# Optimization experiments

Measured on AMD Instinct MI355X. Metric: run time of the kernel, lower is better.

The kernel has to match this reference:

```python
import math
import jax, jax.numpy as jnp
import numpy as np

B, P, L = 32, 128, 64
DIN, TE, H, NH, NL = 16, 64, 512, 8, 2
DH = H // NH
DP = DIN + TE
TAU = 300.0
DELTA = 300.0

_PARAM_SPEC = [
    ("te_scale_w", (1, 1)), ("te_scale_b", (1,)),
    ("te_per_w", (TE - 1, 1)), ("te_per_b", (TE - 1,)),
    ("inp_w", (H, DP)), ("inp_b", (H,)),
    ("wq", (H, H)), ("bq", (H,)), ("wk", (H, H)), ("bk", (H,)),
    ("wv", (H, H)), ("bv", (H,)), ("wo", (H, H)), ("bo", (H,)),
    ("ffn_w1", (H, H)), ("ffn_b1", (H,)), ("ffn_w2", (H, H)), ("ffn_b2", (H,)),
    ("ln1_g", (H,)), ("ln1_b", (H,)), ("ln2_g", (H,)), ("ln2_b", (H,)),
    ("exists_bias", (1, 1, H)),
    ("gwq", (NL, H, H)), ("gbq", (NL, H)), ("gwk", (NL, H, H)), ("gbk", (NL, H)),
    ("gwv", (NL, H, H)), ("gbv", (NL, H)), ("gwo", (NL, H, H)), ("gbo", (NL, H)),
]


def setup_inputs() -> dict:
    key = jax.random.key(0)
    ks = jax.random.split(key, 3 + len(_PARAM_SPEC))
    inp = {
        "x": jax.random.normal(ks[0], (B, P, L, DIN), jnp.float32),
        "tt": jax.random.uniform(ks[1], (B, P, L, 1), jnp.float32),
        "mask": jax.random.randint(ks[2], (B, P, L, 1), 0, 2).astype(jnp.int32),
    }
    for i, (name, shp) in enumerate(_PARAM_SPEC):
        inp[name] = 0.02 * jax.random.normal(ks[3 + i], shp, jnp.float32)
    # LayerNorm affine params: gamma=1, beta=0
    inp["ln1_g"] = jnp.ones((H,), jnp.float32)
    inp["ln1_b"] = jnp.zeros((H,), jnp.float32)
    inp["ln2_g"] = jnp.ones((H,), jnp.float32)
    inp["ln2_b"] = jnp.zeros((H,), jnp.float32)
    return inp


def _layernorm(x, g, b, eps=1e-5):
    m = x.mean(-1, keepdims=True)
    v = ((x - m) ** 2).mean(-1, keepdims=True)
    return (x - m) / jnp.sqrt(v + eps) * g + b


def _time_bias(m):
    idx = jnp.arange(m)
    dist = jnp.abs(idx[:, None] - idx[None, :]).astype(jnp.float32) * DELTA
    return jnp.log(jnp.exp(-dist / TAU) + 1e-12)  # [P, P]


def _pos_encoding(p, d):
    pos = jnp.arange(p, dtype=jnp.float32)[:, None]
    div = jnp.exp(jnp.arange(0, d, 2, dtype=jnp.float32) * (-math.log(10000.0) / d))
    pe = jnp.zeros((p, d), jnp.float32)
    pe = pe.at[:, 0::2].set(jnp.sin(pos * div))
    pe = pe.at[:, 1::2].set(jnp.cos(pos * div))
    return pe


def reference(x, tt, mask,
              te_scale_w, te_scale_b, te_per_w, te_per_b,
              inp_w, inp_b, wq, bq, wk, bk, wv, bv, wo, bo,
              ffn_w1, ffn_b1, ffn_w2, ffn_b2, ln1_g, ln1_b, ln2_g, ln2_b,
              exists_bias, gwq, gbq, gwk, gbk, gwv, gbv, gwo, gbo):
    b, p, l, _ = x.shape
    # --- Learnable time embedding: scale linear + sin(periodic linear), concat ---
    te1 = tt @ te_scale_w.T + te_scale_b                      # [B,P,L,1]
    te2 = jnp.sin(tt @ te_per_w.T + te_per_b)                 # [B,P,L,TE-1]
    pts = jnp.concatenate([x, te1, te2], axis=-1)             # [B,P,L,DP]

    valid = (mask[..., 0] > 0).reshape(b * p, l)              # [N,L] bool
    h = (pts.reshape(b * p, l, DP) @ inp_w.T) + inp_b         # [N,L,H]

    has_any = jnp.any(valid, axis=1)                          # [N]
    key_pad = ~valid
    # Empty patches: unmask position 0 and zero its features
    key_pad = key_pad.at[:, 0].set(key_pad[:, 0] & has_any)
    pos0 = (jnp.arange(l) == 0)[None, :, None]
    h = jnp.where((~has_any)[:, None, None] & pos0, 0.0, h)

    # --- Intra-patch MHA (GAT) ---
    def heads(t, w, bias):
        return ((t @ w.T) + bias).reshape(b * p, l, NH, DH)
    q, k, v = heads(h, wq, bq), heads(h, wk, bk), heads(h, wv, bv)
    sc = jnp.einsum("nqhd,nkhd->nhqk", q, k) / math.sqrt(DH)
    sc = jnp.where(key_pad[:, None, None, :], -1e9, sc)
    z = jnp.einsum("nhqk,nkhd->nqhd", jax.nn.softmax(sc, axis=-1), v)
    z = z.reshape(b * p, l, H) @ wo.T + bo
    h = _layernorm(h + z, ln1_g, ln1_b)
    ffn = jax.nn.relu(h @ ffn_w1.T + ffn_b1) @ ffn_w2.T + ffn_b2
    h = _layernorm(h + ffn, ln2_g, ln2_b)

    # Masked mean pooling -> patch tokens
    w = valid.astype(jnp.float32)[..., None]                  # [N,L,1]
    denom = jnp.clip(w.sum(axis=1), 1.0)
    h = ((h * w).sum(axis=1) / denom).reshape(b, p, H)        # [B,P,H]

    # Exists bias for missing patches + positional encoding
    pexists = has_any.reshape(b, p).astype(jnp.float32)       # [B,P]
    h = h + exists_bias * (1.0 - pexists)[..., None]
    h = h + _pos_encoding(p, H)[None]

    # --- Patch-level time-biased graph attention stack (residual) ---
    tb = _time_bias(p)[None, None]                            # [1,1,P,P]
    kp = (pexists <= 0.0)[:, None, None, :]                   # [B,1,1,P]
    for li in range(NL):
        def gh(t, w, bias):
            return ((t @ w.T) + bias).reshape(b, p, NH, DH)
        q = gh(h, gwq[li], gbq[li])
        k = gh(h, gwk[li], gbk[li])
        v = gh(h, gwv[li], gbv[li])
        att = jnp.einsum("bqhd,bkhd->bhqk", q, k) / math.sqrt(DH) + tb
        att = jnp.where(kp, -1e9, att)
        out = jnp.einsum("bhqk,bkhd->bqhd", jax.nn.softmax(att, axis=-1), v)
        out = out.reshape(b, p, H) @ gwo[li].T + gbo[li]
        out = out * pexists[..., None]
        h = h + out
    return h
```

## Files before the change

### kernel.cpp

```cpp
#include <hip/hip_runtime.h>

#define NTOK 4096
#define CH   512
#define NCHUNK 8

typedef _Float16 f16;
typedef __attribute__((ext_vector_type(8))) _Float16 half8;
typedef __attribute__((ext_vector_type(4))) _Float16 half4;
typedef __attribute__((ext_vector_type(4))) float f32x4;

#define OFF_INPW 0
#define OFF_WQKV (512*128)
#define OFF_WO   (OFF_WQKV + 3*512*512)
#define OFF_W1   (OFF_WO + 512*512)
#define OFF_W2   (OFF_W1 + 512*512)
#define OFF_GW   (OFF_W2 + 512*512)
#define WBF_TOT  (OFF_GW + 8*512*512)

static __device__ __forceinline__ f32x4 mfma16(half8 a, half8 b, f32x4 c){
  return __builtin_amdgcn_mfma_f32_16x16x32_f16(a, b, c, 0, 0, 0);
}

static __device__ __forceinline__ void gld_lds16(const f16* g, f16* l){
  __builtin_amdgcn_global_load_lds(
      (const __attribute__((address_space(1))) void*)g,
      (__attribute__((address_space(3))) void*)l, 16, 0, 0);
}

#define FULL_BARRIER() do { \
    asm volatile("" ::: "memory"); \
    __builtin_amdgcn_s_barrier(); \
    __builtin_amdgcn_sched_barrier(0); \
  } while(0)

__global__ __launch_bounds__(256) void conv_weights(
    const float* __restrict__ inpw, const float* __restrict__ wq, const float* __restrict__ wk,
    const float* __restrict__ wv, const float* __restrict__ wo, const float* __restrict__ w1,
    const float* __restrict__ w2, const float* __restrict__ gwq, const float* __restrict__ gwk,
    const float* __restrict__ gwv, const float* __restrict__ gwo, f16* __restrict__ wbf,
    const float* __restrict__ bq, const float* __restrict__ bk, const float* __restrict__ bv,
    const float* __restrict__ gbq, const float* __restrict__ gbk, const float* __restrict__ gbv,
    float* __restrict__ biasb)
{
  int e = blockIdx.x*256 + threadIdx.x;
  int y = blockIdx.y;
  if (y == 0){
    if (e < 512*128){
      int row = e>>7, col = e&127;
      float v = (col < 80) ? inpw[row*80 + col] : 0.f;
      wbf[OFF_INPW + e] = (f16)v;
    }
    return;
  }
  if (y == 15){
    if (e < 1536){
      biasb[e] = (e < 512) ? bq[e] : (e < 1024 ? bk[e-512] : bv[e-1024]);
    } else if (e < 3*1536){
      int idx = e - 1536, li = idx/1536, c = idx - li*1536;
      float v = (c < 512) ? gbq[li*512 + c] : (c < 1024 ? gbk[li*512 + c-512] : gbv[li*512 + c-1024]);
      biasb[e] = v;
    }
    return;
  }
  if (e >= 512*512) return;
  const float* src; int off;
  if (y <= 6){
    const float* tab[6] = {wq, wk, wv, wo, w1, w2};
    src = tab[y-1]; off = OFF_WQKV + (y-1)*512*512;
  } else {
    int idx = y-7; int li = idx>>2, part = idx&3;
    const float* tab[4] = {gwq, gwk, gwv, gwo};
    src = tab[part] + (size_t)li*512*512; off = OFF_GW + idx*512*512;
  }
  wbf[off + e] = (f16)src[e];
}

__global__ __launch_bounds__(256) void build_mask(
    const int* __restrict__ mask, float* __restrict__ mb, float* __restrict__ pex)
{
  int wv = threadIdx.x>>6, lane = threadIdx.x&63;
  int n = blockIdx.x*4 + wv;
  int valid = mask[(size_t)n*64 + lane] > 0;
  unsigned long long ball = __ballot(valid);
  int hasany = (ball != 0ull);
  int masked = (lane == 0) ? (!valid && hasany) : (!valid);
  mb[(size_t)n*64 + lane] = masked ? -1e9f : 0.f;
  if (lane == 0) pex[n] = hasany ? 1.f : 0.f;
}

__global__ __launch_bounds__(256) void pts_build(
    const float* __restrict__ x, const float* __restrict__ tt,
    const float* __restrict__ tsw, const float* __restrict__ tsb,
    const float* __restrict__ tpw, const float* __restrict__ tpb,
    f16* __restrict__ pts, int rowbase)
{
  int e = blockIdx.x*256 + threadIdx.x;
  int r = e>>7, col = e&127;
  size_t grow = (size_t)rowbase + r;
  float v;
  if (col < 16) v = x[grow*16 + col];
  else if (col >= 80) v = 0.f;
  else {
    float t = tt[grow];
    if (col == 16) v = t*tsw[0] + tsb[0];
    else           v = __sinf(t*tpw[col-17] + tpb[col-17]);
  }
  pts[e] = (f16)v;
}

template<int RESID, bool RELU, bool OUTF32, bool ZEMPTY>
__global__ __launch_bounds__(256) void gemm128(
    const f16* __restrict__ A, const f16* __restrict__ W, const float* __restrict__ bias,
    void* __restrict__ Cout, const void* __restrict__ Rsd, const float* __restrict__ pex,
    int K, int lda, int ldc, int nbase)
{
  __shared__ __align__(16) f16 As[128][64];
  __shared__ __align__(16) f16 Bs[128][64];
  const int tid = threadIdx.x;
  const int m0 = blockIdx.x*128, n0 = blockIdx.y*128;
  const int wv = tid>>6, lane = tid&63, l15 = lane&15, quad = lane>>4;
  const int wm = (wv&1)*64, wn = (wv>>1)*64;
  const int srow = lane>>3;
  const int schunk = (lane&7) ^ srow;
  f32x4 acc[4][4] = {};
  for (int kc = 0; kc < K; kc += 64){
    __syncthreads();
    #pragma unroll
    for (int i=0; i<4; i++){
      const int rA = wv*32 + i*8;
      gld_lds16(A + (size_t)(m0 + rA + srow)*lda + kc + schunk*8, &As[rA][0]);
      gld_lds16(W + (size_t)(n0 + rA + srow)*K   + kc + schunk*8, &Bs[rA][0]);
    }
    __syncthreads();
    #pragma unroll
    for (int kk=0; kk<2; kk++){
      half8 av[4], bv8[4];
      #pragma unroll
      for (int t=0; t<4; t++){
        const int ra = wm + t*16 + l15;
        av[t]  = *(const half8*)(&As[ra][(((kk*4 + quad) ^ (ra&7)))*8]);
        const int rb = wn + t*16 + l15;
        bv8[t] = *(const half8*)(&Bs[rb][(((kk*4 + quad) ^ (rb&7)))*8]);
      }
      #pragma unroll
      for (int mt=0; mt<4; mt++)
        #pragma unroll
        for (int nt=0; nt<4; nt++)
          acc[mt][nt] = mfma16(av[mt], bv8[nt], acc[mt][nt]);
    }
  }
  #pragma unroll
  for (int mt=0; mt<4; mt++){
    #pragma unroll
    for (int nt=0; nt<4; nt++){
      #pragma unroll
      for (int i=0; i<4; i++){
        int gr = m0 + wm + mt*16 + quad*4 + i;
        int gc = n0 + wn + nt*16 + l15;
        float v = acc[mt][nt][i] + bias[gc];
        if (RELU) v = fmaxf(v, 0.f);
        if (RESID == 1) v += (float)((const f16*)Rsd)[(size_t)gr*ldc + gc];
        if (ZEMPTY){ if ((gr&63)==0 && pex[nbase + (gr>>6)]==0.f) v = 0.f; }
        if (RESID == 2) v = v*pex[gr] + ((const float*)Rsd)[(size_t)gr*ldc + gc];
        if (OUTF32) ((float*)Cout)[(size_t)gr*ldc + gc] = v;
        else        ((f16*)Cout)[(size_t)gr*ldc + gc] = (f16)v;
      }
    }
  }
}

template<int RESID, bool RELU>
__global__ __launch_bounds__(512,2) void gemm256(
    const f16* __restrict__ A, const f16* __restrict__ W, const float* __restrict__ bias,
    f16* __restrict__ Cout, const f16* __restrict__ Rsd,
    int K, int lda, int ldc)
{
  __shared__ __align__(16) f16 As[2*2*128*64];
  __shared__ __align__(16) f16 Bs[2*2*128*64];

  const int tid = threadIdx.x;
  const int wv = tid>>6, lane = tid&63, l15 = lane&15, quad = lane>>4;
  const int wm = wv>>2;
  const int wn = wv&3;

  const int gx = gridDim.x, gy = gridDim.y;
  int nwg = gx*gy;
  int orig = blockIdx.x*gy + blockIdx.y;
  int qq = nwg>>3;
  int swz = (orig&7)*qq + (orig>>3);
  const int m0 = (swz/gy)*256, n0 = (swz%gy)*256;

  const int NT = K>>6;

  auto stage_half = [&](int t, int hf){
    int tc = t < NT ? t : NT-1;
    int kc = tc<<6;
    int b  = t & 1;
    #pragma unroll
    for (int i=0;i<2;i++){
      int idx = wv*2+i;
      int row = idx*8 + (lane>>3);
      int col = kc + (((lane&7) ^ (lane>>3))<<3);
      if (hf < 2)
        gld_lds16(A + (size_t)(m0 + hf*128 + row)*lda + col,
                  As + b*16384 + hf*8192 + idx*512);
      else
        gld_lds16(W + (size_t)(n0 + (hf-2)*128 + row)*K + col,
                  Bs + b*16384 + (hf-2)*8192 + idx*512);
    }
  };
  auto ldsA = [&](int b, int mt, int kk)->half8{
    int r = mt*16 + l15;
    int g = kk*4 + quad;
    return *(const half8*)(As + b*16384 + wm*8192 + r*64 + ((g ^ (r&7))<<3));
  };
  auto ldsB = [&](int b, int nt, int kk)->half8{
    int r = (wn&1)*64 + nt*16 + l15;
    int g = kk*4 + quad;
    return *(const half8*)(Bs + b*16384 + (wn>>1)*8192 + r*64 + ((g ^ (r&7))<<3));
  };

  half8 a[8], b0[4], b1[4];
  f32x4 acc[8][4] = {};
  auto mm8 = [&](int mb, half8* bq, int nb){
    __builtin_amdgcn_s_setprio(1);
    #pragma unroll
    for (int m=0;m<4;m++)
      #pragma unroll
      for (int n=0;n<2;n++)
        #pragma unroll
        for (int k=0;k<2;k++)
          acc[mb+m][nb+n] = mfma16(a[m*2+k], bq[n*2+k], acc[mb+m][nb+n]);
    __builtin_amdgcn_s_setprio(0);
  };

  stage_half(0,0); stage_half(0,1); stage_half(0,2); stage_half(0,3);
  stage_half(1,2); stage_half(1,3);
  asm volatile("s_waitcnt vmcnt(4)" ::: "memory");
  FULL_BARRIER();

  for (int t = 0; t < NT; t += 2){
    #pragma unroll
    for (int hv = 0; hv < 2; hv++){
      const int c  = t + hv;
      const int bf = hv;
      #pragma unroll
      for (int m=0;m<4;m++){ a[m*2]=ldsA(bf,m,0); a[m*2+1]=ldsA(bf,m,1); }
      #pragma unroll
      for (int n=0;n<2;n++){ b0[n*2]=ldsB(bf,n,0); b0[n*2+1]=ldsB(bf,n,1); }
      stage_half(c+1, 0);
      FULL_BARRIER();
      mm8(0, b0, 0);
      FULL_BARRIER();
      #pragma unroll
      for (int n=0;n<2;n++){ b1[n*2]=ldsB(bf,n+2,0); b1[n*2+1]=ldsB(bf,n+2,1); }
      stage_half(c+1, 1);
      FULL_BARRIER();
      mm8(0, b1, 2);
      FULL_BARRIER();
      #pragma unroll
      for (int m=0;m<4;m++){ a[m*2]=ldsA(bf,m+4,0); a[m*2+1]=ldsA(bf,m+4,1); }
      stage_half(c+2, 2);
      FULL_BARRIER();
      mm8(4, b1, 2);
      FULL_BARRIER();
      stage_half(c+2, 3);
      asm volatile("s_waitcnt vmcnt(4)" ::: "memory");
      FULL_BARRIER();
      mm8(4, b0, 0);
      FULL_BARRIER();
    }
  }

  #pragma unroll
  for (int mt=0; mt<8; mt++){
    #pragma unroll
    for (int nt=0; nt<4; nt++){
      #pragma unroll
      for (int i=0; i<4; i++){
        int gr = m0 + wm*128 + mt*16 + quad*4 + i;
        int gc = n0 + wn*64  + nt*16 + l15;
        float v = acc[mt][nt][i] + bias[gc];
        if (RELU) v = fmaxf(v, 0.f);
        if (RESID == 1) v += (float)Rsd[(size_t)gr*ldc + gc];
        Cout[(size_t)gr*ldc + gc] = (f16)v;
      }
    }
  }
}

__global__ __launch_bounds__(128) void attn_patch(
    f16* __restrict__ qkv, const float* __restrict__ maskbias, int nbase)
{
  __shared__ f16 Vt[2][64][72];
  __shared__ f16 Ps[2][64][72];
  __shared__ float mbs[64];
  const int tid = threadIdx.x, wv = tid>>6, lane = tid&63, l15 = lane&15, quad = lane>>4;
  const int n = blockIdx.x, h = blockIdx.y*2 + wv;
  if (tid < 64) mbs[tid] = maskbias[(size_t)(nbase+n)*64 + tid];
  const f16* Vb = qkv + 1024 + h*64;
  for (int i=0; i<64; i++)
    Vt[wv][lane][i] = Vb[((size_t)n*64 + i)*1536 + lane];
  __syncthreads();
  const f16* Qb  = qkv + (size_t)n*64*1536 + h*64;
  const f16* Kbb = Qb + 512;
  f32x4 sacc[4][4] = {};
  #pragma unroll
  for (int kc=0; kc<2; kc++){
    half8 af[4], bf[4];
    #pragma unroll
    for (int t4=0; t4<4; t4++){
      af[t4] = *(const half8*)(Qb  + (size_t)(t4*16 + l15)*1536 + kc*32 + quad*8);
      bf[t4] = *(const half8*)(Kbb + (size_t)(t4*16 + l15)*1536 + kc*32 + quad*8);
    }
    #pragma unroll
    for (int ti=0; ti<4; ti++)
      #pragma unroll
      for (int tj=0; tj<4; tj++)
        sacc[ti][tj] = mfma16(af[ti], bf[tj], sacc[ti][tj]);
  }
  #pragma unroll
  for (int ti=0; ti<4; ti++){
    #pragma unroll
    for (int i=0; i<4; i++){
      float mx = -1e30f;
      #pragma unroll
      for (int tj=0; tj<4; tj++){
        float sv = sacc[ti][tj][i]*0.125f + mbs[tj*16 + l15];
        sacc[ti][tj][i] = sv;
        mx = fmaxf(mx, sv);
      }
      #pragma unroll
      for (int off=1; off<16; off<<=1) mx = fmaxf(mx, __shfl_xor(mx, off, 64));
      float sum = 0.f;
      #pragma unroll
      for (int tj=0; tj<4; tj++){
        float pv = __expf(sacc[ti][tj][i] - mx);
        sacc[ti][tj][i] = pv; sum += pv;
      }
      #pragma unroll
      for (int off=1; off<16; off<<=1) sum += __shfl_xor(sum, off, 64);
      float inv = 1.f/sum;
      int q = ti*16 + quad*4 + i;
      #pragma unroll
      for (int tj=0; tj<4; tj++)
        Ps[wv][q][tj*16 + l15] = (f16)(sacc[ti][tj][i]*inv);
    }
  }
  __syncthreads();
  f32x4 zacc[4][4] = {};
  #pragma unroll
  for (int kc=0; kc<2; kc++){
    half8 va[4], pb[4];
    #pragma unroll
    for (int t4=0; t4<4; t4++){
      va[t4] = *(const half8*)(&Vt[wv][t4*16 + l15][kc*32 + quad*8]);
      pb[t4] = *(const half8*)(&Ps[wv][t4*16 + l15][kc*32 + quad*8]);
    }
    #pragma unroll
    for (int ti2=0; ti2<4; ti2++)
      #pragma unroll
      for (int tj=0; tj<4; tj++)
        zacc[ti2][tj] = mfma16(va[ti2], pb[tj], zacc[ti2][tj]);
  }
  __syncthreads();
  #pragma unroll
  for (int ti2=0; ti2<4; ti2++)
    #pragma unroll
    for (int tj=0; tj<4; tj++){
      int q = tj*16 + l15, d0 = ti2*16 + quad*4;
      half4 pk;
      #pragma unroll
      for (int i=0; i<4; i++) pk[i] = (f16)zacc[ti2][tj][i];
      *(half4*)(&Vt[wv][q][d0]) = pk;
    }
  __syncthreads();
  #pragma unroll
  for (int i=0; i<8; i++){
    int q = i*8 + (lane>>3), d0 = (lane&7)*8;
    *(uint4*)(qkv + ((size_t)n*64 + q)*1536 + h*64 + d0) = *(const uint4*)(&Vt[wv][q][d0]);
  }
}

__global__ __launch_bounds__(256) void ln_rows(
    const f16* __restrict__ X, f16* __restrict__ Y,
    const float* __restrict__ g, const float* __restrict__ b)
{
  int wv = threadIdx.x>>6, lane = threadIdx.x&63;
  size_t row = (size_t)blockIdx.x*4 + wv;
  half8 raw = *(const half8*)(X + row*512 + lane*8);
  float xv[8];
  #pragma unroll
  for (int j=0; j<8; j++) xv[j] = (float)raw[j];
  float s = 0.f;
  #pragma unroll
  for (int j=0; j<8; j++) s += xv[j];
  #pragma unroll
  for (int off=1; off<64; off<<=1) s += __shfl_xor(s, off, 64);
  float mean = s*(1.f/512.f);
  float vs = 0.f;
  #pragma unroll
  for (int j=0; j<8; j++){ float d = xv[j]-mean; vs += d*d; }
  #pragma unroll
  for (int off=1; off<64; off<<=1) vs += __shfl_xor(vs, off, 64);
  float rstd = rsqrtf(vs*(1.f/512.f) + 1e-5f);
  half8 o;
  #pragma unroll
  for (int j=0; j<8; j++){
    int c = lane*8 + j;
    o[j] = (f16)((xv[j]-mean)*rstd*g[c] + b[c]);
  }
  *(half8*)(Y + row*512 + lane*8) = o;
}

__global__ __launch_bounds__(256) void pool_ln2(
    const f16* __restrict__ X, const int* __restrict__ mask,
    const float* __restrict__ g, const float* __restrict__ b, const float* __restrict__ eb,
    float* __restrict__ out, int nbase)
{
  __shared__ float mArr[64], rArr[64], vArr[64];
  const int tid = threadIdx.x, wv = tid>>6, lane = tid&63;
  const int n = blockIdx.x, ng = nbase + n, p = ng & 127;
  for (int j=0; j<16; j++){
    int l = wv*16 + j;
    half8 raw = *(const half8*)(X + ((size_t)n*64 + l)*512 + lane*8);
    float s=0.f, ss=0.f;
    #pragma unroll
    for (int jj=0; jj<8; jj++){ float f = (float)raw[jj]; s += f; ss += f*f; }
    #pragma unroll
    for (int off=1; off<64; off<<=1){ s += __shfl_xor(s, off, 64); ss += __shfl_xor(ss, off, 64); }
    if (lane == 0){
      float m = s*(1.f/512.f);
      mArr[l] = m; rArr[l] = rsqrtf(ss*(1.f/512.f) - m*m + 1e-5f);
    }
  }
  if (tid < 64) vArr[tid] = (mask[(size_t)ng*64 + tid] > 0) ? 1.f : 0.f;
  __syncthreads();
  float cnt = 0.f;
  #pragma unroll
  for (int l=0; l<64; l++) cnt += vArr[l];
  float denom = fmaxf(cnt, 1.f);
  float pexv = cnt > 0.f ? 1.f : 0.f;
  float a0=0.f, a1=0.f;
  for (int l=0; l<64; l++){
    float wgt = vArr[l], m = mArr[l], rs = rArr[l];
    float x0 = (float)X[((size_t)n*64+l)*512 + tid];
    float x1 = (float)X[((size_t)n*64+l)*512 + tid + 256];
    a0 += wgt*(x0-m)*rs; a1 += wgt*(x1-m)*rs;
  }
  #pragma unroll
  for (int k=0; k<2; k++){
    int c = tid + k*256;
    float acc = k ? a1 : a0;
    float fr = __expf(-(float)(c & ~1) * (9.210340371976184f/512.f));
    float ang = (float)p * fr;
    float pe = (c & 1) ? cosf(ang) : sinf(ang);
    float o = (g[c]*acc + b[c]*cnt)/denom + eb[c]*(1.f - pexv) + pe;
    out[(size_t)ng*512 + c] = o;
  }
}

__global__ __launch_bounds__(256) void cvt_f32_f16(const float* __restrict__ s, f16* __restrict__ d){
  int i = blockIdx.x*256 + threadIdx.x;
  d[i] = (f16)s[i];
}

__global__ __launch_bounds__(256) void attn_graph(
    f16* __restrict__ qkv, const float* __restrict__ pexists)
{
  __shared__ f16 Vt[64][136];
  __shared__ f16 Ps[4][32][136];
  __shared__ float pxs[128];
  const int tid = threadIdx.x, wv = tid>>6, lane = tid&63, l15 = lane&15, quad = lane>>4;
  const int b = blockIdx.x, h = blockIdx.y;
  if (tid < 128) pxs[tid] = pexists[b*128 + tid];
  const f16* Vb = qkv + 1024 + h*64;
  for (int i=0; i<32; i++){
    int e = tid + i*256, k = e>>6, d = e&63;
    Vt[d][k] = Vb[((size_t)b*128 + k)*1536 + d];
  }
  __syncthreads();
  const f16* Qb = qkv + h*64;
  const f16* Kb = qkv + 512 + h*64;
  const int qb = wv*32;
  f32x4 sacc[2][8] = {};
  #pragma unroll
  for (int kc=0; kc<2; kc++){
    half8 af[2], bf[8];
    #pragma unroll
    for (int ti=0; ti<2; ti++)
      af[ti] = *(const half8*)(Qb + ((size_t)b*128 + qb + ti*16 + l15)*1536 + kc*32 + quad*8);
    #pragma unroll
    for (int tj=0; tj<8; tj++)
      bf[tj] = *(const half8*)(Kb + ((size_t)b*128 + tj*16 + l15)*1536 + kc*32 + quad*8);
    #pragma unroll
    for (int ti=0; ti<2; ti++)
      #pragma unroll
      for (int tj=0; tj<8; tj++)
        sacc[ti][tj] = mfma16(af[ti], bf[tj], sacc[ti][tj]);
  }
  #pragma unroll
  for (int ti=0; ti<2; ti++){
    #pragma unroll
    for (int i=0; i<4; i++){
      int q = qb + ti*16 + quad*4 + i;
      float mx = -1e30f;
      #pragma unroll
      for (int tj=0; tj<8; tj++){
        int col = tj*16 + l15;
        int dd = q - col; if (dd < 0) dd = -dd;
        float tb = __logf(__expf(-(float)dd) + 1e-12f);
        float sv = sacc[ti][tj][i]*0.125f + tb + (pxs[col] > 0.f ? 0.f : -1e9f);
        sacc[ti][tj][i] = sv;
        mx = fmaxf(mx, sv);
      }
      #pragma unroll
      for (int off=1; off<16; off<<=1) mx = fmaxf(mx, __shfl_xor(mx, off, 64));
      float sum = 0.f;
      #pragma unroll
      for (int tj=0; tj<8; tj++){
        float pv = __expf(sacc[ti][tj][i] - mx);
        sacc[ti][tj][i] = pv; sum += pv;
      }
      #pragma unroll
      for (int off=1; off<16; off<<=1) sum += __shfl_xor(sum, off, 64);
      float inv = 1.f/sum;
      int ql = ti*16 + quad*4 + i;
      #pragma unroll
      for (int tj=0; tj<8; tj++)
        Ps[wv][ql][tj*16 + l15] = (f16)(sacc[ti][tj][i]*inv);
    }
  }
  __syncthreads();
  f32x4 zacc[4][2] = {};
  #pragma unroll
  for (int kc=0; kc<4; kc++){
    half8 va[4], pb[2];
    #pragma unroll
    for (int ti2=0; ti2<4; ti2++)
      va[ti2] = *(const half8*)(&Vt[ti2*16 + l15][kc*32 + quad*8]);
    #pragma unroll
    for (int tjq=0; tjq<2; tjq++)
      pb[tjq] = *(const half8*)(&Ps[wv][tjq*16 + l15][kc*32 + quad*8]);
    #pragma unroll
    for (int ti2=0; ti2<4; ti2++)
      #pragma unroll
      for (int tjq=0; tjq<2; tjq++)
        zacc[ti2][tjq] = mfma16(va[ti2], pb[tjq], zacc[ti2][tjq]);
  }
  __syncthreads();
  #pragma unroll
  for (int ti2=0; ti2<4; ti2++)
    #pragma unroll
    for (int tjq=0; tjq<2; tjq++){
      int ql = tjq*16 + l15, d0 = ti2*16 + quad*4;
      half4 pk;
      #pragma unroll
      for (int i=0; i<4; i++) pk[i] = (f16)zacc[ti2][tjq][i];
      *(half4*)(&Ps[wv][ql][d0]) = pk;
    }
  __syncthreads();
  {
    int q = tid>>1, hf = tid&1;
    const f16* src = &Ps[q>>5][q&31][hf*32];
    #pragma unroll
    for (int j=0; j<4; j++)
      *(uint4*)(qkv + ((size_t)b*128 + q)*1536 + h*64 + hf*32 + j*8) = *(const uint4*)(src + j*8);
  }
}

extern "C" void kernel_launch(void* const* d_in, const int* in_sizes, int n_in,
                              void* d_out, int out_size, void* d_ws, size_t ws_size,
                              hipStream_t stream)
{
  (void)in_sizes; (void)n_in; (void)out_size; (void)ws_size;
  const float* x    = (const float*)d_in[0];
  const float* tt   = (const float*)d_in[1];
  const int*   mask = (const int*)  d_in[2];
  const float* tsw  = (const float*)d_in[3];
  const float* tsb  = (const float*)d_in[4];
  const float* tpw  = (const float*)d_in[5];
  const float* tpb  = (const float*)d_in[6];
  const float* inpw = (const float*)d_in[7];
  const float* inpb = (const float*)d_in[8];
  const float* wq   = (const float*)d_in[9];
  const float* bq   = (const float*)d_in[10];
  const float* wk   = (const float*)d_in[11];
  const float* bk   = (const float*)d_in[12];
  const float* wv   = (const float*)d_in[13];
  const float* bv   = (const float*)d_in[14];
  const float* wo   = (const float*)d_in[15];
  const float* bo   = (const float*)d_in[16];
  const float* w1   = (const float*)d_in[17];
  const float* b1   = (const float*)d_in[18];
  const float* w2   = (const float*)d_in[19];
  const float* b2   = (const float*)d_in[20];
  const float* ln1g = (const float*)d_in[21];
  const float* ln1b = (const float*)d_in[22];
  const float* ln2g = (const float*)d_in[23];
  const float* ln2b = (const float*)d_in[24];
  const float* eb   = (const float*)d_in[25];
  const float* gwq  = (const float*)d_in[26];
  const float* gbq  = (const float*)d_in[27];
  const float* gwk  = (const float*)d_in[28];
  const float* gbk  = (const float*)d_in[29];
  const float* gwv  = (const float*)d_in[30];
  const float* gbv  = (const float*)d_in[31];
  const float* gwo  = (const float*)d_in[32];
  const float* gbo  = (const float*)d_in[33];
  float* out = (float*)d_out;

  char* wp = (char*)d_ws;
  auto alloc = [&](size_t bytes)->char*{
    char* p = wp; wp += (bytes + 255) & ~(size_t)255; return p;
  };
  f16*   wbf   = (f16*)  alloc((size_t)WBF_TOT*2);
  float* mb    = (float*)alloc((size_t)NTOK*64*4);
  float* pex   = (float*)alloc((size_t)NTOK*4);
  float* biasb = (float*)alloc((size_t)3*1536*4);
  f16*   ptsb  = (f16*)  alloc((size_t)CH*64*128*2);
  f16*   bufA  = (f16*)  alloc((size_t)CH*64*512*2);
  f16*   bufB  = (f16*)  alloc((size_t)CH*64*512*2);
  f16*   bufC  = (f16*)  alloc((size_t)CH*64*512*2);
  f16*   qkv   = (f16*)  alloc((size_t)CH*64*1536*2);

  conv_weights<<<dim3(1024,16),256,0,stream>>>(inpw,wq,wk,wv,wo,w1,w2,gwq,gwk,gwv,gwo,wbf,
                                               bq,bk,bv,gbq,gbk,gbv,biasb);
  build_mask<<<NTOK/4,256,0,stream>>>(mask, mb, pex);

  const int MB  = CH*64/128;
  const int MB2 = CH*64/256;
  for (int ch=0; ch<NCHUNK; ch++){
    int nbase = ch*CH;
    int rowbase = nbase*64;
    pts_build<<<CH*64*128/256,256,0,stream>>>(x,tt,tsw,tsb,tpw,tpb,ptsb,rowbase);
    gemm128<0,false,false,true ><<<dim3(MB,4),256,0,stream>>>(ptsb, wbf+OFF_INPW, inpb, bufA, nullptr, pex, 128, 128, 512, nbase);
    gemm256<0,false><<<dim3(MB2,6),512,0,stream>>>(bufA, wbf+OFF_WQKV, biasb, qkv, nullptr, 512, 512, 1536);
    attn_patch<<<dim3(CH,4),128,0,stream>>>(qkv, mb, nbase);
    gemm256<1,false><<<dim3(MB2,2),512,0,stream>>>(qkv, wbf+OFF_WO, bo, bufA, bufA, 512, 1536, 512);
    ln_rows<<<CH*64/4,256,0,stream>>>(bufA, bufB, ln1g, ln1b);
    gemm256<0,true ><<<dim3(MB2,2),512,0,stream>>>(bufB, wbf+OFF_W1, b1, bufC, nullptr, 512, 512, 512);
    gemm256<1,false><<<dim3(MB2,2),512,0,stream>>>(bufC, wbf+OFF_W2, b2, bufB, bufB, 512, 512, 512);
    pool_ln2<<<CH,256,0,stream>>>(bufB, mask, ln2g, ln2b, eb, out, nbase);
  }

  f16* hbf  = bufA;
  f16* qkvg = bufB;
  for (int li=0; li<2; li++){
    cvt_f32_f16<<<NTOK*512/256,256,0,stream>>>(out, hbf);
    gemm128<0,false,false,false><<<dim3(32,12),256,0,stream>>>(hbf, wbf+OFF_GW + (size_t)li*4*512*512, biasb + 1536*(1+li), qkvg, nullptr, nullptr, 512, 512, 1536, 0);
    attn_graph<<<dim3(32,8),256,0,stream>>>(qkvg, pex);
    gemm128<2,false,true ,false><<<dim3(32,4),256,0,stream>>>(qkvg, wbf+OFF_GW + (size_t)(li*4+3)*512*512, gbo+li*512, out, out, pex, 512, 1536, 512, 0);
  }
}
```

Before: 2.276 ms.

## Fuse LayerNorms and pooling into full-row GEMM epilogues, drop conversion kernels

Adds a GEMM kernel where one block computes all 512 output columns of 128 rows, so LayerNorm statistics can be reduced inside the block. The Wo GEMM now applies residual plus LN1 in its epilogue, and the W2 GEMM applies residual, LN2, masked mean pooling, exists bias and positional encoding, writing the f32 output and an f16 copy. The graph-stage output GEMM also writes the f16 copy, so the separate ln_rows, pool_ln2 and cvt kernels and their HBM round trips disappear. The trade-off is fewer, larger blocks (32 per chunk) with high register use, which lowers parallelism for these GEMMs.

```diff
diff --git a/kernel.cpp b/kernel.cpp
--- a/kernel.cpp
+++ b/kernel.cpp
@@ -112,7 +112,7 @@
 __global__ __launch_bounds__(256) void gemm128(
     const f16* __restrict__ A, const f16* __restrict__ W, const float* __restrict__ bias,
     void* __restrict__ Cout, const void* __restrict__ Rsd, const float* __restrict__ pex,
-    int K, int lda, int ldc, int nbase)
+    int K, int lda, int ldc, int nbase, f16* __restrict__ dual)
 {
   __shared__ __align__(16) f16 As[128][64];
   __shared__ __align__(16) f16 Bs[128][64];
@@ -164,6 +164,7 @@
         if (RESID == 2) v = v*pex[gr] + ((const float*)Rsd)[(size_t)gr*ldc + gc];
         if (OUTF32) ((float*)Cout)[(size_t)gr*ldc + gc] = v;
         else        ((f16*)Cout)[(size_t)gr*ldc + gc] = (f16)v;
+        if (RESID == 2){ if (dual) dual[(size_t)gr*ldc + gc] = (f16)v; }
       }
     }
   }
@@ -289,6 +290,159 @@
   }
 }
 
+template<int EPI>
+__global__ __launch_bounds__(512,2) void gemm_row512(
+    const f16* __restrict__ A, const f16* __restrict__ W, const float* __restrict__ bias,
+    f16* __restrict__ Cf16, const f16* __restrict__ Rsd,
+    const float* __restrict__ g, const float* __restrict__ be,
+    const float* __restrict__ eb, const int* __restrict__ mask,
+    float* __restrict__ outp, f16* __restrict__ hcopy,
+    int lda, int nbase)
+{
+  __shared__ __align__(16) f16 As[128][64];
+  __shared__ __align__(16) f16 Bs[512][64];
+  __shared__ float stS[128][4], stQ[128][4];
+  __shared__ float vArr[128];
+
+  const int tid = threadIdx.x;
+  const int wv = tid>>6, lane = tid&63, l15 = lane&15, quad = lane>>4;
+  const int wm = wv>>2, wn = wv&3;
+  const int m0 = blockIdx.x*128;
+  const int srow = lane>>3;
+  const int schunk = (lane&7) ^ srow;
+
+  if (EPI == 2){
+    if (tid < 128){
+      int ngt = nbase + blockIdx.x*2 + (tid>>6);
+      vArr[tid] = (mask[(size_t)ngt*64 + (tid&63)] > 0) ? 1.f : 0.f;
+    }
+  }
+
+  f32x4 acc[4][8] = {};
+  for (int kc = 0; kc < 512; kc += 64){
+    __syncthreads();
+    #pragma unroll
+    for (int i=0; i<2; i++){
+      const int rA = wv*16 + i*8;
+      gld_lds16(A + (size_t)(m0 + rA + srow)*lda + kc + schunk*8, &As[rA][0]);
+    }
+    #pragma unroll
+    for (int i=0; i<8; i++){
+      const int rB = wv*64 + i*8;
+      gld_lds16(W + (size_t)(rB + srow)*512 + kc + schunk*8, &Bs[rB][0]);
+    }
+    __syncthreads();
+    #pragma unroll
+    for (int kk=0; kk<2; kk++){
+      half8 a[4], b[8];
+      #pragma unroll
+      for (int mt=0; mt<4; mt++){
+        const int ra = wm*64 + mt*16 + l15;
+        a[mt] = *(const half8*)(&As[ra][(((kk*4 + quad) ^ (ra&7)))*8]);
+      }
+      #pragma unroll
+      for (int nt=0; nt<8; nt++){
+        const int rb = wn*128 + nt*16 + l15;
+        b[nt] = *(const half8*)(&Bs[rb][(((kk*4 + quad) ^ (rb&7)))*8]);
+      }
+      #pragma unroll
+      for (int mt=0; mt<4; mt++)
+        #pragma unroll
+        for (int nt=0; nt<8; nt++)
+          acc[mt][nt] = mfma16(a[mt], b[nt], acc[mt][nt]);
+    }
+  }
+
+  #pragma unroll
+  for (int nt=0; nt<8; nt++){
+    int c = wn*128 + nt*16 + l15;
+    float bv = bias[c];
+    #pragma unroll
+    for (int mt=0; mt<4; mt++)
+      #pragma unroll
+      for (int i=0; i<4; i++){
+        int gr = m0 + wm*64 + mt*16 + quad*4 + i;
+        acc[mt][nt][i] += bv + (float)Rsd[(size_t)gr*512 + c];
+      }
+  }
+  #pragma unroll
+  for (int mt=0; mt<4; mt++)
+    #pragma unroll
+    for (int i=0; i<4; i++){
+      float s = 0.f, sq = 0.f;
+      #pragma unroll
+      for (int nt=0; nt<8; nt++){ float v = acc[mt][nt][i]; s += v; sq += v*v; }
+      #pragma unroll
+      for (int off=1; off<16; off<<=1){ s += __shfl_xor(s, off, 64); sq += __shfl_xor(sq, off, 64); }
+      if (l15 == 0){
+        int r = wm*64 + mt*16 + quad*4 + i;
+        stS[r][wn] = s; stQ[r][wn] = sq;
+      }
+    }
+  __syncthreads();
+  float m_[4][4], rs_[4][4];
+  #pragma unroll
+  for (int mt=0; mt<4; mt++)
+    #pragma unroll
+    for (int i=0; i<4; i++){
+      int r = wm*64 + mt*16 + quad*4 + i;
+      float ts = stS[r][0] + stS[r][1] + stS[r][2] + stS[r][3];
+      float tq = stQ[r][0] + stQ[r][1] + stQ[r][2] + stQ[r][3];
+      float m = ts*(1.f/512.f);
+      m_[mt][i] = m;
+      rs_[mt][i] = rsqrtf(tq*(1.f/512.f) - m*m + 1e-5f);
+    }
+
+  if (EPI == 1){
+    #pragma unroll
+    for (int nt=0; nt<8; nt++){
+      int c = wn*128 + nt*16 + l15;
+      float gc_ = g[c], bec = be[c];
+      #pragma unroll
+      for (int mt=0; mt<4; mt++)
+        #pragma unroll
+        for (int i=0; i<4; i++){
+          int gr = m0 + wm*64 + mt*16 + quad*4 + i;
+          Cf16[(size_t)gr*512 + c] = (f16)((acc[mt][nt][i] - m_[mt][i])*rs_[mt][i]*gc_ + bec);
+        }
+    }
+  } else {
+    float wA[4][4];
+    #pragma unroll
+    for (int mt=0; mt<4; mt++)
+      #pragma unroll
+      for (int i=0; i<4; i++)
+        wA[mt][i] = vArr[wm*64 + mt*16 + quad*4 + i];
+    float cnt = 0.f;
+    #pragma unroll
+    for (int l=0; l<64; l++) cnt += vArr[wm*64 + l];
+    float denom = fmaxf(cnt, 1.f);
+    float pexv = cnt > 0.f ? 1.f : 0.f;
+    int ng = nbase + blockIdx.x*2 + wm;
+    int pidx = ng & 127;
+    #pragma unroll
+    for (int nt=0; nt<8; nt++){
+      int c = wn*128 + nt*16 + l15;
+      float p = 0.f;
+      #pragma unroll
+      for (int mt=0; mt<4; mt++)
+        #pragma unroll
+        for (int i=0; i<4; i++)
+          p += wA[mt][i]*(acc[mt][nt][i] - m_[mt][i])*rs_[mt][i];
+      p += __shfl_xor(p, 16, 64);
+      p += __shfl_xor(p, 32, 64);
+      if (quad == 0){
+        float fr = __expf(-(float)(c & ~1) * (9.210340371976184f/512.f));
+        float ang = (float)pidx * fr;
+        float pe = (c & 1) ? cosf(ang) : sinf(ang);
+        float o = (g[c]*p + be[c]*cnt)/denom + eb[c]*(1.f - pexv) + pe;
+        outp[(size_t)ng*512 + c] = o;
+        hcopy[(size_t)ng*512 + c] = (f16)o;
+      }
+    }
+  }
+}
+
 __global__ __launch_bounds__(128) void attn_patch(
     f16* __restrict__ qkv, const float* __restrict__ maskbias, int nbase)
 {
@@ -380,89 +534,6 @@
     int q = i*8 + (lane>>3), d0 = (lane&7)*8;
     *(uint4*)(qkv + ((size_t)n*64 + q)*1536 + h*64 + d0) = *(const uint4*)(&Vt[wv][q][d0]);
   }
-}
-
-__global__ __launch_bounds__(256) void ln_rows(
-    const f16* __restrict__ X, f16* __restrict__ Y,
-    const float* __restrict__ g, const float* __restrict__ b)
-{
-  int wv = threadIdx.x>>6, lane = threadIdx.x&63;
-  size_t row = (size_t)blockIdx.x*4 + wv;
-  half8 raw = *(const half8*)(X + row*512 + lane*8);
-  float xv[8];
-  #pragma unroll
-  for (int j=0; j<8; j++) xv[j] = (float)raw[j];
-  float s = 0.f;
-  #pragma unroll
-  for (int j=0; j<8; j++) s += xv[j];
-  #pragma unroll
-  for (int off=1; off<64; off<<=1) s += __shfl_xor(s, off, 64);
-  float mean = s*(1.f/512.f);
-  float vs = 0.f;
-  #pragma unroll
-  for (int j=0; j<8; j++){ float d = xv[j]-mean; vs += d*d; }
-  #pragma unroll
-  for (int off=1; off<64; off<<=1) vs += __shfl_xor(vs, off, 64);
-  float rstd = rsqrtf(vs*(1.f/512.f) + 1e-5f);
-  half8 o;
-  #pragma unroll
-  for (int j=0; j<8; j++){
-    int c = lane*8 + j;
-    o[j] = (f16)((xv[j]-mean)*rstd*g[c] + b[c]);
-  }
-  *(half8*)(Y + row*512 + lane*8) = o;
-}
-
-__global__ __launch_bounds__(256) void pool_ln2(
-    const f16* __restrict__ X, const int* __restrict__ mask,
-    const float* __restrict__ g, const float* __restrict__ b, const float* __restrict__ eb,
-    float* __restrict__ out, int nbase)
-{
-  __shared__ float mArr[64], rArr[64], vArr[64];
-  const int tid = threadIdx.x, wv = tid>>6, lane = tid&63;
-  const int n = blockIdx.x, ng = nbase + n, p = ng & 127;
-  for (int j=0; j<16; j++){
-    int l = wv*16 + j;
-    half8 raw = *(const half8*)(X + ((size_t)n*64 + l)*512 + lane*8);
-    float s=0.f, ss=0.f;
-    #pragma unroll
-    for (int jj=0; jj<8; jj++){ float f = (float)raw[jj]; s += f; ss += f*f; }
-    #pragma unroll
-    for (int off=1; off<64; off<<=1){ s += __shfl_xor(s, off, 64); ss += __shfl_xor(ss, off, 64); }
-    if (lane == 0){
-      float m = s*(1.f/512.f);
-      mArr[l] = m; rArr[l] = rsqrtf(ss*(1.f/512.f) - m*m + 1e-5f);
-    }
-  }
-  if (tid < 64) vArr[tid] = (mask[(size_t)ng*64 + tid] > 0) ? 1.f : 0.f;
-  __syncthreads();
-  float cnt = 0.f;
-  #pragma unroll
-  for (int l=0; l<64; l++) cnt += vArr[l];
-  float denom = fmaxf(cnt, 1.f);
-  float pexv = cnt > 0.f ? 1.f : 0.f;
-  float a0=0.f, a1=0.f;
-  for (int l=0; l<64; l++){
-    float wgt = vArr[l], m = mArr[l], rs = rArr[l];
-    float x0 = (float)X[((size_t)n*64+l)*512 + tid];
-    float x1 = (float)X[((size_t)n*64+l)*512 + tid + 256];
-    a0 += wgt*(x0-m)*rs; a1 += wgt*(x1-m)*rs;
-  }
-  #pragma unroll
-  for (int k=0; k<2; k++){
-    int c = tid + k*256;
-    float acc = k ? a1 : a0;
-    float fr = __expf(-(float)(c & ~1) * (9.210340371976184f/512.f));
-    float ang = (float)p * fr;
-    float pe = (c & 1) ? cosf(ang) : sinf(ang);
-    float o = (g[c]*acc + b[c]*cnt)/denom + eb[c]*(1.f - pexv) + pe;
-    out[(size_t)ng*512 + c] = o;
-  }
-}
-
-__global__ __launch_bounds__(256) void cvt_f32_f16(const float* __restrict__ s, f16* __restrict__ d){
-  int i = blockIdx.x*256 + threadIdx.x;
-  d[i] = (f16)s[i];
 }
 
 __global__ __launch_bounds__(256) void attn_graph(
@@ -623,6 +694,7 @@
   f16*   bufB  = (f16*)  alloc((size_t)CH*64*512*2);
   f16*   bufC  = (f16*)  alloc((size_t)CH*64*512*2);
   f16*   qkv   = (f16*)  alloc((size_t)CH*64*1536*2);
+  f16*   hbf   = (f16*)  alloc((size_t)NTOK*512*2);
 
   conv_weights<<<dim3(1024,16),256,0,stream>>>(inpw,wq,wk,wv,wo,w1,w2,gwq,gwk,gwv,gwo,wbf,
                                                bq,bk,bv,gbq,gbk,gbv,biasb);
@@ -630,26 +702,25 @@
 
   const int MB  = CH*64/128;
   const int MB2 = CH*64/256;
+  const int MBR = CH*64/128;
   for (int ch=0; ch<NCHUNK; ch++){
     int nbase = ch*CH;
     int rowbase = nbase*64;
     pts_build<<<CH*64*128/256,256,0,stream>>>(x,tt,tsw,tsb,tpw,tpb,ptsb,rowbase);
-    gemm128<0,false,false,true ><<<dim3(MB,4),256,0,stream>>>(ptsb, wbf+OFF_INPW, inpb, bufA, nullptr, pex, 128, 128, 512, nbase);
+    gemm128<0,false,false,true ><<<dim3(MB,4),256,0,stream>>>(ptsb, wbf+OFF_INPW, inpb, bufA, nullptr, pex, 128, 128, 512, nbase, nullptr);
     gemm256<0,false><<<dim3(MB2,6),512,0,stream>>>(bufA, wbf+OFF_WQKV, biasb, qkv, nullptr, 512, 512, 1536);
     attn_patch<<<dim3(CH,4),128,0,stream>>>(qkv, mb, nbase);
-    gemm256<1,false><<<dim3(MB2,2),512,0,stream>>>(qkv, wbf+OFF_WO, bo, bufA, bufA, 512, 1536, 512);
-    ln_rows<<<CH*64/4,256,0,stream>>>(bufA, bufB, ln1g, ln1b);
+    gemm_row512<1><<<MBR,512,0,stream>>>(qkv, wbf+OFF_WO, bo, bufB, bufA,
+                                         ln1g, ln1b, nullptr, nullptr, nullptr, nullptr, 1536, nbase);
     gemm256<0,true ><<<dim3(MB2,2),512,0,stream>>>(bufB, wbf+OFF_W1, b1, bufC, nullptr, 512, 512, 512);
-    gemm256<1,false><<<dim3(MB2,2),512,0,stream>>>(bufC, wbf+OFF_W2, b2, bufB, bufB, 512, 512, 512);
-    pool_ln2<<<CH,256,0,stream>>>(bufB, mask, ln2g, ln2b, eb, out, nbase);
-  }
-
-  f16* hbf  = bufA;
+    gemm_row512<2><<<MBR,512,0,stream>>>(bufC, wbf+OFF_W2, b2, nullptr, bufB,
+                                         ln2g, ln2b, eb, mask, out, hbf, 512, nbase);
+  }
+
   f16* qkvg = bufB;
   for (int li=0; li<2; li++){
-    cvt_f32_f16<<<NTOK*512/256,256,0,stream>>>(out, hbf);
-    gemm128<0,false,false,false><<<dim3(32,12),256,0,stream>>>(hbf, wbf+OFF_GW + (size_t)li*4*512*512, biasb + 1536*(1+li), qkvg, nullptr, nullptr, 512, 512, 1536, 0);
+    gemm128<0,false,false,false><<<dim3(32,12),256,0,stream>>>(hbf, wbf+OFF_GW + (size_t)li*4*512*512, biasb + 1536*(1+li), qkvg, nullptr, nullptr, 512, 512, 1536, 0, nullptr);
     attn_graph<<<dim3(32,8),256,0,stream>>>(qkvg, pex);
-    gemm128<2,false,true ,false><<<dim3(32,4),256,0,stream>>>(qkvg, wbf+OFF_GW + (size_t)(li*4+3)*512*512, gbo+li*512, out, out, pex, 512, 1536, 512, 0);
-  }
-}
+    gemm128<2,false,true ,false><<<dim3(32,4),256,0,stream>>>(qkvg, wbf+OFF_GW + (size_t)(li*4+3)*512*512, gbo+li*512, out, out, pex, 512, 1536, 512, 0, (li==0)? hbf : nullptr);
+  }
+}
```

Measured after the change: 2.502 ms. 1.1x slower.
